# Kernel optimization log

Measured on AMD Instinct MI355X. Metric: run time of the kernel, lower is better.

The kernel has to match this reference:

```python
import jax, jax.numpy as jnp
import numpy as np
import math

B, C, H, W = 16, 512, 32, 32
GROUPS = 32
EPS = 1e-5


def group_norm(x, w, b):
    # x: [B, C, H, W]; normalize within each of GROUPS channel groups over (C//G, H, W)
    Bx, Cx, Hx, Wx = x.shape
    xg = x.reshape(Bx, GROUPS, Cx // GROUPS, Hx, Wx)
    mean = xg.mean(axis=(2, 3, 4), keepdims=True)
    var = xg.var(axis=(2, 3, 4), keepdims=True)
    xg = (xg - mean) * jax.lax.rsqrt(var + EPS)
    xn = xg.reshape(Bx, Cx, Hx, Wx)
    return xn * w[None, :, None, None] + b[None, :, None, None]


def setup_inputs() -> dict:
    key = jax.random.key(0)
    ks = jax.random.split(key, 4)
    x = jax.random.normal(ks[0], (B, C, H, W), dtype=jnp.float32)
    gn_w = jnp.ones((C,), dtype=jnp.float32)
    gn_b = jnp.zeros((C,), dtype=jnp.float32)
    # Conv2d 1x1 weights as [out, in] matrices; PyTorch default init scale
    qkv_w = jax.random.normal(ks[1], (3 * C, C), dtype=jnp.float32) * (1.0 / math.sqrt(C))
    qkv_b = jnp.zeros((3 * C,), dtype=jnp.float32)
    out_w = jax.random.normal(ks[2], (C, C), dtype=jnp.float32) * (1.0 / math.sqrt(C))
    out_b = jnp.zeros((C,), dtype=jnp.float32)
    return {"x": x, "gn_w": gn_w, "gn_b": gn_b, "qkv_w": qkv_w,
            "qkv_b": qkv_b, "out_w": out_w, "out_b": out_b}


def reference(x, gn_w, gn_b, qkv_w, qkv_b, out_w, out_b):
    Bx, Cx, Hx, Wx = x.shape
    N = Hx * Wx
    h = group_norm(x, gn_w, gn_b)                       # [B, C, H, W]
    hf = h.reshape(Bx, Cx, N)                           # [B, C, N]
    # 1x1 conv == channel matmul
    qkv = jnp.einsum('oc,bcn->bon', qkv_w, hf) + qkv_b[None, :, None]  # [B, 3C, N]
    q, k, v = jnp.split(qkv, 3, axis=1)                 # each [B, C, N]
    q = q.transpose(0, 2, 1)                            # [B, N, C]
    v = v.transpose(0, 2, 1)                            # [B, N, C]
    scale = 1.0 / math.sqrt(Cx)
    attn = jnp.einsum('bnc,bcm->bnm', q, k) * scale     # [B, N, N]
    attn = jax.nn.softmax(attn, axis=-1)
    o = jnp.einsum('bnm,bmc->bnc', attn, v)             # [B, N, C]
    o = o.transpose(0, 2, 1)                            # [B, C, N]
    o = jnp.einsum('oc,bcn->bon', out_w, o) + out_b[None, :, None]
    return x + o.reshape(Bx, Cx, Hx, Wx)
```

## Files before the change

### kernel.cpp

```cpp
#include <hip/hip_runtime.h>

typedef unsigned short u16;
typedef short short8 __attribute__((ext_vector_type(8)));
typedef float floatx4 __attribute__((ext_vector_type(4)));
typedef u16 u16x4 __attribute__((ext_vector_type(4)));
typedef u16 u16x8 __attribute__((ext_vector_type(8)));

#define DEVI __device__ __forceinline__

DEVI u16 f2bf(float x) {
    union { float f; unsigned u; } c; c.f = x;
    unsigned u = c.u;
    u += 0x7fffu + ((u >> 16) & 1u);
    return (u16)(u >> 16);
}
DEVI float bf2f(u16 h) {
    union { unsigned u; float f; } c; c.u = ((unsigned)h) << 16;
    return c.f;
}

DEVI void gload_lds16(const void* g, void* l) {
    auto gp = (const __attribute__((address_space(1))) unsigned*)(unsigned long long)g;
    auto lp = (__attribute__((address_space(3))) unsigned*)(unsigned)(unsigned long long)l;
    __builtin_amdgcn_global_load_lds(gp, lp, 16, 0, 0);
}

__global__ __launch_bounds__(256) void gn_fused_kernel(const float* __restrict__ x,
                                                       const float* __restrict__ w,
                                                       const float* __restrict__ bb,
                                                       u16* __restrict__ h) {
    const int bg = blockIdx.x;
    const int b = bg >> 5, g = bg & 31;
    const float* xg = x + (long long)bg * 16384;
    const float4* p4 = (const float4*)xg;
    float s = 0.f, s2 = 0.f;
    #pragma unroll
    for (int i = 0; i < 16; i++) {
        float4 v = p4[threadIdx.x + i * 256];
        s  += v.x + v.y + v.z + v.w;
        s2 += v.x*v.x + v.y*v.y + v.z*v.z + v.w*v.w;
    }
    #pragma unroll
    for (int m = 1; m < 64; m <<= 1) { s += __shfl_xor(s, m, 64); s2 += __shfl_xor(s2, m, 64); }
    __shared__ float rs[4], rq[4];
    if ((threadIdx.x & 63) == 0) { rs[threadIdx.x >> 6] = s; rq[threadIdx.x >> 6] = s2; }
    __syncthreads();
    float mean = (rs[0] + rs[1] + rs[2] + rs[3]) * (1.f / 16384.f);
    float var  = (rq[0] + rq[1] + rq[2] + rq[3]) * (1.f / 16384.f) - mean * mean;
    float rstd = rsqrtf(var + 1e-5f);

    float sc[16], sh[16];
    #pragma unroll
    for (int cc = 0; cc < 16; cc++) {
        int c = g * 16 + cc;
        sc[cc] = w[c] * rstd;
        sh[cc] = bb[c] - mean * sc[cc];
    }
    const int n0 = threadIdx.x * 4;
    u16x8 o[4][2];
    #pragma unroll
    for (int cc = 0; cc < 16; cc++) {
        float4 xv = *(const float4*)&xg[cc * 1024 + n0];
        o[0][cc >> 3][cc & 7] = f2bf(xv.x * sc[cc] + sh[cc]);
        o[1][cc >> 3][cc & 7] = f2bf(xv.y * sc[cc] + sh[cc]);
        o[2][cc >> 3][cc & 7] = f2bf(xv.z * sc[cc] + sh[cc]);
        o[3][cc >> 3][cc & 7] = f2bf(xv.w * sc[cc] + sh[cc]);
    }
    u16* hb = h + ((long long)b * 1024 + n0) * 512 + g * 16;
    #pragma unroll
    for (int k = 0; k < 4; k++) {
        *(u16x8*)&hb[(long long)k * 512]     = o[k][0];
        *(u16x8*)&hb[(long long)k * 512 + 8] = o[k][1];
    }
}

__global__ __launch_bounds__(256) void f2bf_kernel(const float* __restrict__ in,
                                                   u16* __restrict__ out, int n) {
    int i = blockIdx.x * 256 + threadIdx.x;
    if (i < n) out[i] = f2bf(in[i]);
}

__global__ __launch_bounds__(256) void softmax_kernel(u16* __restrict__ P) {
    const int wave = threadIdx.x >> 6, lane = threadIdx.x & 63;
    const long long row = (long long)blockIdx.x * 4 + wave;
    u16* p = P + row * 1024 + lane * 16;
    u16x8 a = *(u16x8*)p;
    u16x8 b = *(u16x8*)(p + 8);
    float v[16];
    #pragma unroll
    for (int k = 0; k < 8; k++) { v[k] = bf2f(a[k]); v[8+k] = bf2f(b[k]); }
    float mx = v[0];
    #pragma unroll
    for (int k = 1; k < 16; k++) mx = fmaxf(mx, v[k]);
    #pragma unroll
    for (int m = 1; m < 64; m <<= 1) mx = fmaxf(mx, __shfl_xor(mx, m, 64));
    float s = 0.f;
    #pragma unroll
    for (int k = 0; k < 16; k++) { v[k] = __expf(v[k] - mx); s += v[k]; }
    #pragma unroll
    for (int m = 1; m < 64; m <<= 1) s += __shfl_xor(s, m, 64);
    float inv = 1.f / s;
    #pragma unroll
    for (int k = 0; k < 8; k++) { a[k] = f2bf(v[k]*inv); b[k] = f2bf(v[8+k]*inv); }
    *(u16x8*)p = a;
    *(u16x8*)(p + 8) = b;
}

template <int MODE>
__global__ __launch_bounds__(256, 3)
void gemm_bt_kernel(const u16* __restrict__ A, const u16* __restrict__ Bt,
                    void* __restrict__ C0, void* __restrict__ C1,
                    const float* __restrict__ bias, const float* __restrict__ res,
                    float scale, int lda, int ldb, int ldc,
                    long long sA, long long sB, long long sC, long long sR, int K) {
    const int t    = threadIdx.x;
    const int lane = t & 63;
    const int wave = t >> 6;
    const int m0   = blockIdx.y * 128;
    const int n0   = blockIdx.x * 128;
    const int z    = blockIdx.z;
    A  += (long long)z * sA;
    Bt += (long long)z * sB;

    __shared__ __align__(16) u16 smem[16384];
    u16* As = smem;
    u16* Bs = smem + 8192;

    const int wm = wave >> 1, wn = wave & 1;
    const int quad = lane >> 4, lrow = lane & 15;

    floatx4 acc[4][4];
    #pragma unroll
    for (int i = 0; i < 4; i++)
        #pragma unroll
        for (int j = 0; j < 4; j++)
            #pragma unroll
            for (int r = 0; r < 4; r++) acc[i][j][r] = 0.f;

    const int rowA = t >> 2;
    const int kch  = (t & 3) * 8;
    const u16* Ag = A  + (long long)(m0 + rowA) * lda + kch;
    const u16* Bg = Bt + (long long)(n0 + rowA) * ldb + kch;
    u16* Al = &As[t * 8];
    u16* Bl = &Bs[t * 8];
    const long long a64 = (long long)64 * lda;
    const long long b64 = (long long)64 * ldb;

    for (int k0 = 0; k0 < K; k0 += 64) {
        gload_lds16(Ag + k0,            Al);
        gload_lds16(Ag + k0 + a64,      Al + 2048);
        gload_lds16(Ag + k0 + 32,       Al + 4096);
        gload_lds16(Ag + k0 + 32 + a64, Al + 6144);
        gload_lds16(Bg + k0,            Bl);
        gload_lds16(Bg + k0 + b64,      Bl + 2048);
        gload_lds16(Bg + k0 + 32,       Bl + 4096);
        gload_lds16(Bg + k0 + 32 + b64, Bl + 6144);
        __syncthreads();
        #pragma unroll
        for (int kk = 0; kk < 2; kk++) {
            short8 af[4], bfr[4];
            #pragma unroll
            for (int i = 0; i < 4; i++)
                af[i] = *(const short8*)&As[kk*4096 + (wm*64 + i*16 + lrow)*32 + quad*8];
            #pragma unroll
            for (int j = 0; j < 4; j++)
                bfr[j] = *(const short8*)&Bs[kk*4096 + (wn*64 + j*16 + lrow)*32 + quad*8];
            #pragma unroll
            for (int i = 0; i < 4; i++)
                #pragma unroll
                for (int j = 0; j < 4; j++)
                    acc[i][j] = __builtin_amdgcn_mfma_f32_16x16x32_bf16(af[i], bfr[j], acc[i][j], 0, 0, 0);
        }
        __syncthreads();
    }

    const int ST = 136;

    if (MODE == 1 || (MODE == 2 && m0 >= 1024)) {
        #pragma unroll
        for (int p = 0; p < 4; p++) {
            if (p) __syncthreads();
            if (wm == (p >> 1)) {
                #pragma unroll
                for (int ii = 0; ii < 2; ii++) {
                    const int i = (p & 1) * 2 + ii;
                    const int row = ii * 16 + quad * 4;
                    #pragma unroll
                    for (int j = 0; j < 4; j++) {
                        const int cB = wn * 64 + j * 16 + lrow;
                        #pragma unroll
                        for (int r = 0; r < 4; r++) {
                            float v = acc[i][j][r] * (MODE == 1 ? scale : 1.0f);
                            if (MODE == 2) v += bias[m0 + p * 32 + row + r];
                            smem[(row + r) * ST + cB] = f2bf(v);
                        }
                    }
                }
            }
            __syncthreads();
            const int rr = t >> 3, cc = (t & 7) * 16;
            u16x8 a0 = *(u16x8*)&smem[rr * ST + cc];
            u16x8 a1 = *(u16x8*)&smem[rr * ST + cc + 8];
            u16* Cp;
            if (MODE == 1)
                Cp = (u16*)C0 + (long long)z * sC + (long long)(m0 + p * 32 + rr) * ldc + n0 + cc;
            else
                Cp = (u16*)C1 + (long long)(m0 - 1024 + p * 32 + rr) * 16384 + n0 + cc;
            *(u16x8*)Cp = a0;
            *(u16x8*)(Cp + 8) = a1;
        }
    } else if (MODE == 2) {
        #pragma unroll
        for (int p = 0; p < 4; p++) {
            if (p) __syncthreads();
            if (wn == (p >> 1)) {
                #pragma unroll
                for (int jj = 0; jj < 2; jj++) {
                    const int j = (p & 1) * 2 + jj;
                    const int row = jj * 16 + lrow;
                    #pragma unroll
                    for (int i = 0; i < 4; i++) {
                        const int mmL = wm * 64 + i * 16 + quad * 4;
                        u16x4 pk;
                        #pragma unroll
                        for (int r = 0; r < 4; r++)
                            pk[r] = f2bf(acc[i][j][r] + bias[m0 + mmL + r]);
                        *(u16x4*)&smem[row * ST + mmL] = pk;
                    }
                }
            }
            __syncthreads();
            const int rr = t >> 3, cc = (t & 7) * 16;
            u16x8 a0 = *(u16x8*)&smem[rr * ST + cc];
            u16x8 a1 = *(u16x8*)&smem[rr * ST + cc + 8];
            u16* Cp = (u16*)C0 + (long long)(n0 + p * 32 + rr) * 1024 + m0 + cc;
            *(u16x8*)Cp = a0;
            *(u16x8*)(Cp + 8) = a1;
        }
    } else {
        float* smf = (float*)smem;
        const int SF = 132;
        float* C = (float*)C0 + (long long)z * sC;
        const float* rz = res + (long long)z * sR;
        #pragma unroll
        for (int p = 0; p < 8; p++) {
            if (p) __syncthreads();
            if (wm == (p >> 2)) {
                const int i = p & 3;
                #pragma unroll
                for (int j = 0; j < 4; j++) {
                    const int cB = wn * 64 + j * 16 + lrow;
                    #pragma unroll
                    for (int r = 0; r < 4; r++)
                        smf[(quad * 4 + r) * SF + cB] =
                            acc[i][j][r] + bias[m0 + p * 16 + quad * 4 + r];
                }
            }
            __syncthreads();
            const int rr = t >> 4, cc = (t & 15) * 8;
            const long long gro = (long long)(m0 + p * 16 + rr) * ldc + n0 + cc;
            float4 rv0 = *(const float4*)&rz[gro];
            float4 rv1 = *(const float4*)&rz[gro + 4];
            float4 ov0, ov1;
            ov0.x = smf[rr*SF + cc + 0] + rv0.x;
            ov0.y = smf[rr*SF + cc + 1] + rv0.y;
            ov0.z = smf[rr*SF + cc + 2] + rv0.z;
            ov0.w = smf[rr*SF + cc + 3] + rv0.w;
            ov1.x = smf[rr*SF + cc + 4] + rv1.x;
            ov1.y = smf[rr*SF + cc + 5] + rv1.y;
            ov1.z = smf[rr*SF + cc + 6] + rv1.z;
            ov1.w = smf[rr*SF + cc + 7] + rv1.w;
            *(float4*)&C[gro]     = ov0;
            *(float4*)&C[gro + 4] = ov1;
        }
    }
}

extern "C" void kernel_launch(void* const* d_in, const int* in_sizes, int n_in,
                              void* d_out, int out_size, void* d_ws, size_t ws_size,
                              hipStream_t stream) {
    (void)in_sizes; (void)n_in; (void)out_size; (void)ws_size;
    const float* x     = (const float*)d_in[0];
    const float* gn_w  = (const float*)d_in[1];
    const float* gn_b  = (const float*)d_in[2];
    const float* qkv_w = (const float*)d_in[3];
    const float* qkv_b = (const float*)d_in[4];
    const float* out_w = (const float*)d_in[5];
    const float* out_b = (const float*)d_in[6];
    float* out = (float*)d_out;

    char* ws = (char*)d_ws;
    u16*  h_t   = (u16*)ws;  ws += (size_t)16*1024*512*2;
    u16*  qkv_t = (u16*)ws;  ws += (size_t)16*1024*1024*2;
    u16*  v2    = (u16*)ws;  ws += (size_t)512*16384*2;
    u16*  S     = (u16*)ws;  ws += (size_t)16*1024*1024*2;
    u16*  O     = (u16*)ws;  ws += (size_t)16*1024*512*2;
    u16*  wq    = (u16*)ws;  ws += (size_t)1536*512*2;
    u16*  wo    = (u16*)ws;  ws += (size_t)512*512*2;

    f2bf_kernel<<<(1536*512 + 255)/256, 256, 0, stream>>>(qkv_w, wq, 1536*512);
    f2bf_kernel<<<(512*512 + 255)/256, 256, 0, stream>>>(out_w, wo, 512*512);
    gn_fused_kernel<<<512, 256, 0, stream>>>(x, gn_w, gn_b, h_t);

    gemm_bt_kernel<2><<<dim3(128, 12, 1), 256, 0, stream>>>(
        wq, h_t, qkv_t, v2, qkv_b, nullptr, 1.0f,
        512, 512, 1024, 0, 0, 0, 0, 512);

    gemm_bt_kernel<1><<<dim3(8, 8, 16), 256, 0, stream>>>(
        qkv_t, qkv_t + 512, S, nullptr, nullptr, nullptr, 0.044194173824159216f,
        1024, 1024, 1024,
        (long long)1024*1024, (long long)1024*1024, (long long)1024*1024, 0, 512);

    softmax_kernel<<<4096, 256, 0, stream>>>(S);

    gemm_bt_kernel<1><<<dim3(4, 8, 16), 256, 0, stream>>>(
        S, v2, O, nullptr, nullptr, nullptr, 1.0f,
        1024, 16384, 512,
        (long long)1024*1024, 1024, (long long)1024*512, 0, 1024);

    gemm_bt_kernel<0><<<dim3(8, 4, 16), 256, 0, stream>>>(
        wo, O, out, nullptr, out_b, x, 1.0f,
        512, 512, 1024,
        0, (long long)1024*512, (long long)512*1024, (long long)512*1024, 512);
}
```

Baseline: 234.1 us.

## Fold output projection into V before attention, dropping the P·V intermediate

```diff
diff --git a/kernel.cpp b/kernel.cpp
--- a/kernel.cpp
+++ b/kernel.cpp
@@ -32,13 +32,15 @@
     const int bg = blockIdx.x;
     const int b = bg >> 5, g = bg & 31;
     const float* xg = x + (long long)bg * 16384;
-    const float4* p4 = (const float4*)xg;
+    const int n0 = threadIdx.x * 4;
+
+    float4 xv[16];
     float s = 0.f, s2 = 0.f;
     #pragma unroll
-    for (int i = 0; i < 16; i++) {
-        float4 v = p4[threadIdx.x + i * 256];
-        s  += v.x + v.y + v.z + v.w;
-        s2 += v.x*v.x + v.y*v.y + v.z*v.z + v.w*v.w;
+    for (int cc = 0; cc < 16; cc++) {
+        xv[cc] = *(const float4*)&xg[cc * 1024 + n0];
+        s  += xv[cc].x + xv[cc].y + xv[cc].z + xv[cc].w;
+        s2 += xv[cc].x*xv[cc].x + xv[cc].y*xv[cc].y + xv[cc].z*xv[cc].z + xv[cc].w*xv[cc].w;
     }
     #pragma unroll
     for (int m = 1; m < 64; m <<= 1) { s += __shfl_xor(s, m, 64); s2 += __shfl_xor(s2, m, 64); }
@@ -49,22 +51,16 @@
     float var  = (rq[0] + rq[1] + rq[2] + rq[3]) * (1.f / 16384.f) - mean * mean;
     float rstd = rsqrtf(var + 1e-5f);
 
-    float sc[16], sh[16];
+    u16x8 o[4][2];
     #pragma unroll
     for (int cc = 0; cc < 16; cc++) {
         int c = g * 16 + cc;
-        sc[cc] = w[c] * rstd;
-        sh[cc] = bb[c] - mean * sc[cc];
-    }
-    const int n0 = threadIdx.x * 4;
-    u16x8 o[4][2];
-    #pragma unroll
-    for (int cc = 0; cc < 16; cc++) {
-        float4 xv = *(const float4*)&xg[cc * 1024 + n0];
-        o[0][cc >> 3][cc & 7] = f2bf(xv.x * sc[cc] + sh[cc]);
-        o[1][cc >> 3][cc & 7] = f2bf(xv.y * sc[cc] + sh[cc]);
-        o[2][cc >> 3][cc & 7] = f2bf(xv.z * sc[cc] + sh[cc]);
-        o[3][cc >> 3][cc & 7] = f2bf(xv.w * sc[cc] + sh[cc]);
+        float sc = w[c] * rstd;
+        float sh = bb[c] - mean * sc;
+        o[0][cc >> 3][cc & 7] = f2bf(xv[cc].x * sc + sh);
+        o[1][cc >> 3][cc & 7] = f2bf(xv[cc].y * sc + sh);
+        o[2][cc >> 3][cc & 7] = f2bf(xv[cc].z * sc + sh);
+        o[3][cc >> 3][cc & 7] = f2bf(xv[cc].w * sc + sh);
     }
     u16* hb = h + ((long long)b * 1024 + n0) * 512 + g * 16;
     #pragma unroll
@@ -74,10 +70,15 @@
     }
 }
 
-__global__ __launch_bounds__(256) void f2bf_kernel(const float* __restrict__ in,
-                                                   u16* __restrict__ out, int n) {
+__global__ __launch_bounds__(256) void wconv_kernel(const float* __restrict__ w1, u16* __restrict__ o1,
+                                                    const float* __restrict__ w2, u16* __restrict__ o2) {
     int i = blockIdx.x * 256 + threadIdx.x;
-    if (i < n) out[i] = f2bf(in[i]);
+    const float* src; u16* dst; int j;
+    if (i < 196608) { src = w1; dst = o1; j = i; }
+    else            { src = w2; dst = o2; j = i - 196608; }
+    float4 v = *(const float4*)&src[j * 4];
+    u16x4 p; p[0] = f2bf(v.x); p[1] = f2bf(v.y); p[2] = f2bf(v.z); p[3] = f2bf(v.w);
+    *(u16x4*)&dst[j * 4] = p;
 }
 
 __global__ __launch_bounds__(256) void softmax_kernel(u16* __restrict__ P) {
@@ -109,7 +110,7 @@
 template <int MODE>
 __global__ __launch_bounds__(256, 3)
 void gemm_bt_kernel(const u16* __restrict__ A, const u16* __restrict__ Bt,
-                    void* __restrict__ C0, void* __restrict__ C1,
+                    void* __restrict__ C0,
                     const float* __restrict__ bias, const float* __restrict__ res,
                     float scale, int lda, int ldb, int ldc,
                     long long sA, long long sB, long long sC, long long sR, int K) {
@@ -176,7 +177,7 @@
 
     const int ST = 136;
 
-    if (MODE == 1 || (MODE == 2 && m0 >= 1024)) {
+    if (MODE == 1) {
         #pragma unroll
         for (int p = 0; p < 4; p++) {
             if (p) __syncthreads();
@@ -189,11 +190,8 @@
                     for (int j = 0; j < 4; j++) {
                         const int cB = wn * 64 + j * 16 + lrow;
                         #pragma unroll
-                        for (int r = 0; r < 4; r++) {
-                            float v = acc[i][j][r] * (MODE == 1 ? scale : 1.0f);
-                            if (MODE == 2) v += bias[m0 + p * 32 + row + r];
-                            smem[(row + r) * ST + cB] = f2bf(v);
-                        }
+                        for (int r = 0; r < 4; r++)
+                            smem[(row + r) * ST + cB] = f2bf(acc[i][j][r] * scale);
                     }
                 }
             }
@@ -201,11 +199,7 @@
             const int rr = t >> 3, cc = (t & 7) * 16;
             u16x8 a0 = *(u16x8*)&smem[rr * ST + cc];
             u16x8 a1 = *(u16x8*)&smem[rr * ST + cc + 8];
-            u16* Cp;
-            if (MODE == 1)
-                Cp = (u16*)C0 + (long long)z * sC + (long long)(m0 + p * 32 + rr) * ldc + n0 + cc;
-            else
-                Cp = (u16*)C1 + (long long)(m0 - 1024 + p * 32 + rr) * 16384 + n0 + cc;
+            u16* Cp = (u16*)C0 + (long long)z * sC + (long long)(m0 + p * 32 + rr) * ldc + n0 + cc;
             *(u16x8*)Cp = a0;
             *(u16x8*)(Cp + 8) = a1;
         }
@@ -233,7 +227,7 @@
             const int rr = t >> 3, cc = (t & 7) * 16;
             u16x8 a0 = *(u16x8*)&smem[rr * ST + cc];
             u16x8 a1 = *(u16x8*)&smem[rr * ST + cc + 8];
-            u16* Cp = (u16*)C0 + (long long)(n0 + p * 32 + rr) * 1024 + m0 + cc;
+            u16* Cp = (u16*)C0 + (long long)(n0 + p * 32 + rr) * ldc + m0 + cc;
             *(u16x8*)Cp = a0;
             *(u16x8*)(Cp + 8) = a1;
         }
@@ -291,35 +285,32 @@
 
     char* ws = (char*)d_ws;
     u16*  h_t   = (u16*)ws;  ws += (size_t)16*1024*512*2;
-    u16*  qkv_t = (u16*)ws;  ws += (size_t)16*1024*1024*2;
-    u16*  v2    = (u16*)ws;  ws += (size_t)512*16384*2;
+    u16*  qkv_t = (u16*)ws;  ws += (size_t)16*1024*1536*2;
+    u16*  vprm  = (u16*)ws;  ws += (size_t)512*16384*2;
     u16*  S     = (u16*)ws;  ws += (size_t)16*1024*1024*2;
-    u16*  O     = (u16*)ws;  ws += (size_t)16*1024*512*2;
     u16*  wq    = (u16*)ws;  ws += (size_t)1536*512*2;
     u16*  wo    = (u16*)ws;  ws += (size_t)512*512*2;
 
-    f2bf_kernel<<<(1536*512 + 255)/256, 256, 0, stream>>>(qkv_w, wq, 1536*512);
-    f2bf_kernel<<<(512*512 + 255)/256, 256, 0, stream>>>(out_w, wo, 512*512);
+    wconv_kernel<<<1024, 256, 0, stream>>>(qkv_w, wq, out_w, wo);
     gn_fused_kernel<<<512, 256, 0, stream>>>(x, gn_w, gn_b, h_t);
 
     gemm_bt_kernel<2><<<dim3(128, 12, 1), 256, 0, stream>>>(
-        wq, h_t, qkv_t, v2, qkv_b, nullptr, 1.0f,
-        512, 512, 1024, 0, 0, 0, 0, 512);
+        wq, h_t, qkv_t, qkv_b, nullptr, 1.0f,
+        512, 512, 1536, 0, 0, 0, 0, 512);
+
+    gemm_bt_kernel<1><<<dim3(128, 4, 1), 256, 0, stream>>>(
+        wo, qkv_t + 1024, vprm, nullptr, nullptr, 1.0f,
+        512, 1536, 16384, 0, 0, 0, 0, 512);
 
     gemm_bt_kernel<1><<<dim3(8, 8, 16), 256, 0, stream>>>(
-        qkv_t, qkv_t + 512, S, nullptr, nullptr, nullptr, 0.044194173824159216f,
-        1024, 1024, 1024,
-        (long long)1024*1024, (long long)1024*1024, (long long)1024*1024, 0, 512);
+        qkv_t, qkv_t + 512, S, nullptr, nullptr, 0.044194173824159216f,
+        1536, 1536, 1024,
+        (long long)1024*1536, (long long)1024*1536, (long long)1024*1024, 0, 512);
 
     softmax_kernel<<<4096, 256, 0, stream>>>(S);
 
-    gemm_bt_kernel<1><<<dim3(4, 8, 16), 256, 0, stream>>>(
-        S, v2, O, nullptr, nullptr, nullptr, 1.0f,
-        1024, 16384, 512,
-        (long long)1024*1024, 1024, (long long)1024*512, 0, 1024);
-
     gemm_bt_kernel<0><<<dim3(8, 4, 16), 256, 0, stream>>>(
-        wo, O, out, nullptr, out_b, x, 1.0f,
-        512, 512, 1024,
-        0, (long long)1024*512, (long long)512*1024, (long long)512*1024, 512);
-}
+        vprm, S, out, out_b, x, 1.0f,
+        16384, 1024, 1024,
+        1024, (long long)1024*1024, (long long)512*1024, (long long)512*1024, 1024);
+}
```

Result: no change. 231.2 us (-1.3%).
